# Performance work log

Hardware: AMD Instinct MI355X
Metric: run time of the kernel (lower is better)

Reference implementation:

```python
import jax, jax.numpy as jnp
from jax import lax
import numpy as np

T, B, I, H, OUT = 1024, 32, 128, 512, 10


def _lstm_layer(x, W_ih, W_hh, b):
    """PyTorch-convention LSTM layer. x: [T,B,in], W_ih: [4H,in], W_hh: [4H,H], b: [4H].
    Gate order: i, f, g, o. Returns all hidden states [T,B,H]."""
    hdim = W_hh.shape[1]
    # Precompute input projections for all timesteps (big GEMM, compute-bound).
    x_proj = jnp.einsum('tbi,gi->tbg', x, W_ih) + b  # [T,B,4H]

    def step(carry, xp_t):
        h, c = carry
        gates = xp_t + h @ W_hh.T  # [B,4H]
        i_g, f_g, g_g, o_g = jnp.split(gates, 4, axis=-1)
        i_g = jax.nn.sigmoid(i_g)
        f_g = jax.nn.sigmoid(f_g)
        g_g = jnp.tanh(g_g)
        o_g = jax.nn.sigmoid(o_g)
        c = f_g * c + i_g * g_g
        h = o_g * jnp.tanh(c)
        return (h, c), h

    h0 = jnp.zeros((x.shape[1], hdim), x.dtype)
    c0 = jnp.zeros((x.shape[1], hdim), x.dtype)
    _, hs = lax.scan(step, (h0, c0), x_proj)
    return hs  # [T,B,H]


def setup_inputs() -> dict:
    key = jax.random.key(0)
    ks = jax.random.split(key, 9)
    s1 = 1.0 / np.sqrt(H)  # PyTorch LSTM init scale U(-1/sqrt(H), 1/sqrt(H)); use scaled normal
    return {
        'data': jax.random.normal(ks[0], (T, B, I), jnp.float32),
        'W_ih1': jax.random.normal(ks[1], (4 * H, I), jnp.float32) * s1,
        'W_hh1': jax.random.normal(ks[2], (4 * H, H), jnp.float32) * s1,
        'b1': jax.random.normal(ks[3], (4 * H,), jnp.float32) * s1,
        'W_ih2': jax.random.normal(ks[4], (4 * H, H), jnp.float32) * s1,
        'W_hh2': jax.random.normal(ks[5], (4 * H, H), jnp.float32) * s1,
        'b2': jax.random.normal(ks[6], (4 * H,), jnp.float32) * s1,
        'W3': jax.random.normal(ks[7], (OUT, H), jnp.float32) * s1,
        'b3': jax.random.normal(ks[8], (OUT,), jnp.float32) * s1,
    }


def reference(data, W_ih1, W_hh1, b1, W_ih2, W_hh2, b2, W3, b3):
    h = _lstm_layer(data, W_ih1, W_hh1, b1)   # [T,B,H]
    h = _lstm_layer(h, W_ih2, W_hh2, b2)      # [T,B,H]
    logits = jnp.einsum('tbh,oh->tbo', h, W3) + b3  # [T,B,OUT]
    return jax.nn.softmax(logits, axis=2)
```

## Files before the change

### kernel.cpp

```cpp
#include <hip/hip_runtime.h>
#include <cstdint>
#include <cstddef>

#define TCHUNK 128
#define NCHUNK 8
#define BATCH 32
#define IDIM 128
#define HDIM 512
#define GDIM 2048
#define ODIM 10
#define NBLK 256
#define XPSTEP (GDIM * BATCH)
#define SLAB_F 16384
#define SLAB_B (SLAB_F * 4)

typedef float f4 __attribute__((ext_vector_type(4)));
typedef float f2 __attribute__((ext_vector_type(2)));

__device__ __forceinline__ void llc_store(float* p, float v) {
  asm volatile("global_store_dword %0, %1, off sc0 sc1" :: "v"(p), "v"(v) : "memory");
}
__device__ __forceinline__ float quad_sum(float x) {
  int t = __builtin_amdgcn_update_dpp(0, __float_as_int(x), 0xB1, 0xF, 0xF, true);
  x += __int_as_float(t);
  t = __builtin_amdgcn_update_dpp(0, __float_as_int(x), 0x4E, 0xF, 0xF, true);
  x += __int_as_float(t);
  return x;
}

#define BARRIER() do {                                                      \
    asm volatile("s_waitcnt lgkmcnt(0)" ::: "memory");                      \
    __builtin_amdgcn_sched_barrier(0);                                      \
    __builtin_amdgcn_s_barrier();                                           \
    __builtin_amdgcn_sched_barrier(0);                                      \
  } while (0)

template<int K>
__launch_bounds__(256, 2)
__global__ void proj_kernel(const float* __restrict__ X,
                            const float* __restrict__ W,
                            const float* __restrict__ bias,
                            float* __restrict__ P) {
  __shared__ float Xs[8][132];
  __shared__ float Ws[8][132];
  const int tid = threadIdx.x;
  const int n0 = blockIdx.x * 128;
  const int m0 = blockIdx.y * 128;
  const int tx = tid & 15, ty = tid >> 4;
  const int lm = tid >> 1;
  const int kq = (tid & 1) * 4;
  f2 acc2[8][4];
#pragma unroll
  for (int i = 0; i < 8; ++i)
#pragma unroll
    for (int j = 0; j < 4; ++j) acc2[i][j] = (f2){0.f, 0.f};

  for (int k0 = 0; k0 < K; k0 += 8) {
    const float4 xv = *(const float4*)&X[(size_t)(m0 + lm) * K + k0 + kq];
    const float4 wv = *(const float4*)&W[(size_t)(n0 + lm) * K + k0 + kq];
    __syncthreads();
    Xs[kq + 0][lm] = xv.x; Xs[kq + 1][lm] = xv.y; Xs[kq + 2][lm] = xv.z; Xs[kq + 3][lm] = xv.w;
    Ws[kq + 0][lm] = wv.x; Ws[kq + 1][lm] = wv.y; Ws[kq + 2][lm] = wv.z; Ws[kq + 3][lm] = wv.w;
    __syncthreads();
#pragma unroll
    for (int kk = 0; kk < 8; ++kk) {
      float a[8];
      *(float4*)&a[0] = *(const float4*)&Xs[kk][ty * 8];
      *(float4*)&a[4] = *(const float4*)&Xs[kk][ty * 8 + 4];
      f2 b2[4];
#pragma unroll
      for (int jp = 0; jp < 4; ++jp) b2[jp] = *(const f2*)&Ws[kk][tx * 8 + 2 * jp];
#pragma unroll
      for (int i = 0; i < 8; ++i)
#pragma unroll
        for (int jp = 0; jp < 4; ++jp) acc2[i][jp] += b2[jp] * a[i];
    }
  }
  const int mb = m0 + ty * 8;
  const int t  = mb >> 5;
  const int b0 = mb & 31;
#pragma unroll
  for (int j = 0; j < 8; ++j) {
    const int n = n0 + tx * 8 + j;
    const float bj = bias[n];
    float* dst = &P[((size_t)t * GDIM + n) * BATCH + b0];
#pragma unroll
    for (int i = 0; i < 8; ++i)
      dst[i] = ((j & 1) ? acc2[i][j >> 1].y : acc2[i][j >> 1].x) + bj;
  }
}

__launch_bounds__(256, 1)
__global__ void scan_kernel(const float* __restrict__ xp,
                            const float* __restrict__ Whh,
                            float* __restrict__ hout,
                            float* __restrict__ hb,
                            float* __restrict__ ccur,
                            int first) {
  __shared__ float h_s[2048];
  __shared__ float red[1024];
  __shared__ float pad[17408];

  const int tid = threadIdx.x, bid = blockIdx.x;
  const int g = bid & 7, rank = bid >> 3, slot16 = rank * 16;
  const int w = tid >> 6, l = tid & 63;
  const int s4 = l & 3, rq = l >> 2;
  const int sg = 4 * w + s4;
  const int kb = 32 * sg;

  float wreg[4][32];
#pragma unroll
  for (int r = 0; r < 4; ++r) {
    const int rl = 4 * rq + r;
    const float* wp = Whh + (size_t)((rl >> 4) * HDIM + slot16 + (rl & 15)) * HDIM + kb;
#pragma unroll
    for (int q8 = 0; q8 < 8; ++q8) {
      const f4 v = *(const f4*)&wp[q8 * 4];
      wreg[r][q8 * 4 + 0] = v.x; wreg[r][q8 * 4 + 1] = v.y;
      wreg[r][q8 * 4 + 2] = v.z; wreg[r][q8 * 4 + 3] = v.w;
    }
  }

  const int cl = l >> 4, m = l & 15;
  const int sgS = 4 * w + (m >> 2);
  int dsaddr[8];
#pragma unroll
  for (int i = 0; i < 8; ++i) {
    const int kk = 8 * (m & 3) + i;
    dsaddr[i] = 128 * sgS + ((4 * kk + 8 * sgS) & 127) + cl;
  }
  const int srcoff = cl * 512 + 128 * w + 8 * m;

  const int jj = l >> 2, bb = l & 3;
  const float* xq = xp + (size_t)(slot16 + jj) * BATCH + g * 4 + bb;

  float c_st = 0.f;
  if (!first && w == 0) c_st = ccur[(size_t)(g * 4 + bb) * HDIM + slot16 + jj];

  const int hb0 = 128 * sg;
  const int rot = (8 * sg) & 127;

#pragma unroll 1
  for (int tt = 0; tt < TCHUNK; ++tt) {
    float xq4[4];
    if (w == 0) {
#pragma unroll
      for (int q = 0; q < 4; ++q)
        xq4[q] = xq[(size_t)tt * XPSTEP + q * (HDIM * BATCH)];
    }
    const float* src = hb + (size_t)tt * SLAB_F + g * 2048 + srcoff;
    f4 va, vb;
    int guard = 0;
    while (true) {
      asm volatile("global_load_dwordx4 %0, %2, off sc0 sc1\n\t"
                   "global_load_dwordx4 %1, %3, off sc0 sc1\n\t"
                   "s_waitcnt vmcnt(0)"
                   : "=&v"(va), "=&v"(vb) : "v"(src), "v"(src + 4) : "memory");
      const bool ok =
          __float_as_uint(va.x) != 0xFFFFFFFFu && __float_as_uint(va.y) != 0xFFFFFFFFu &&
          __float_as_uint(va.z) != 0xFFFFFFFFu && __float_as_uint(va.w) != 0xFFFFFFFFu &&
          __float_as_uint(vb.x) != 0xFFFFFFFFu && __float_as_uint(vb.y) != 0xFFFFFFFFu &&
          __float_as_uint(vb.z) != 0xFFFFFFFFu && __float_as_uint(vb.w) != 0xFFFFFFFFu;
      if (__all(ok) || ++guard > 100000) break;
      __builtin_amdgcn_s_sleep(1);
    }
    h_s[dsaddr[0]] = va.x; h_s[dsaddr[1]] = va.y;
    h_s[dsaddr[2]] = va.z; h_s[dsaddr[3]] = va.w;
    h_s[dsaddr[4]] = vb.x; h_s[dsaddr[5]] = vb.y;
    h_s[dsaddr[6]] = vb.z; h_s[dsaddr[7]] = vb.w;
    BARRIER();

    f2 a01[4], a23[4];
#pragma unroll
    for (int r = 0; r < 4; ++r) { a01[r] = (f2){0.f, 0.f}; a23[r] = (f2){0.f, 0.f}; }
#pragma unroll
    for (int kk = 0; kk < 32; ++kk) {
      const f4 hv = *(const f4*)&h_s[hb0 + ((4 * kk + rot) & 127)];
      const f2 h01 = {hv.x, hv.y}, h23 = {hv.z, hv.w};
#pragma unroll
      for (int r = 0; r < 4; ++r) {
        a01[r] += h01 * wreg[r][kk];
        a23[r] += h23 * wreg[r][kk];
      }
    }
#pragma unroll
    for (int r = 0; r < 4; ++r) {
      a01[r].x = quad_sum(a01[r].x); a01[r].y = quad_sum(a01[r].y);
      a23[r].x = quad_sum(a23[r].x); a23[r].y = quad_sum(a23[r].y);
    }
    f2 r01, r23;
    { const f2 v0 = (s4 & 1) ? a01[1] : a01[0];
      const f2 v1 = (s4 & 1) ? a01[3] : a01[2];
      r01 = (s4 & 2) ? v1 : v0;
      const f2 u0 = (s4 & 1) ? a23[1] : a23[0];
      const f2 u1 = (s4 & 1) ? a23[3] : a23[2];
      r23 = (s4 & 2) ? u1 : u0; }
    *(f4*)&red[(w << 8) + 4 * l] = (f4){r01.x, r01.y, r23.x, r23.y};
    BARRIER();

    if (w == 0) {
      float pre[4];
#pragma unroll
      for (int q = 0; q < 4; ++q) {
        const int ri = 4 * (16 * q + jj) + bb;
        pre[q] = red[ri] + red[256 + ri] + red[512 + ri] + red[768 + ri] + xq4[q];
      }
      const float ig = 1.f / (1.f + __expf(-pre[0]));
      const float fg = 1.f / (1.f + __expf(-pre[1]));
      const float gg = tanhf(pre[2]);
      const float og = 1.f / (1.f + __expf(-pre[3]));
      c_st = fg * c_st + ig * gg;
      const float hval = og * tanhf(c_st);
      llc_store(hb + (size_t)(tt + 1) * SLAB_F + g * 2048 + bb * 512 + slot16 + jj, hval);
      hout[(size_t)tt * (BATCH * HDIM) + (size_t)(g * 4 + bb) * HDIM + slot16 + jj] = hval;
    }
  }
  if (w == 0) ccur[(size_t)(g * 4 + bb) * HDIM + slot16 + jj] = c_st;
  ((volatile float*)pad)[tid] = c_st;
}

__launch_bounds__(256, 2)
__global__ void head_kernel(const float* __restrict__ h2,
                            const float* __restrict__ W3,
                            const float* __restrict__ b3,
                            float* __restrict__ outp) {
  const int tid = threadIdx.x;
  const int lane = tid & 63;
  const int wv = tid >> 6;
  const int row = blockIdx.x * 4 + wv;
  const float* hrow = &h2[(size_t)row * HDIM];
  float hreg[8];
  *(float4*)&hreg[0] = *(const float4*)&hrow[lane * 8];
  *(float4*)&hreg[4] = *(const float4*)&hrow[lane * 8 + 4];
  float logit[ODIM];
#pragma unroll
  for (int o = 0; o < ODIM; ++o) {
    const float* wrow = &W3[o * HDIM + lane * 8];
    float w[8];
    *(float4*)&w[0] = *(const float4*)&wrow[0];
    *(float4*)&w[4] = *(const float4*)&wrow[4];
    float pp = 0.f;
#pragma unroll
    for (int j = 0; j < 8; ++j) pp += hreg[j] * w[j];
#pragma unroll
    for (int off = 32; off > 0; off >>= 1) pp += __shfl_xor(pp, off);
    logit[o] = pp + b3[o];
  }
  float mx = logit[0];
#pragma unroll
  for (int o = 1; o < ODIM; ++o) mx = fmaxf(mx, logit[o]);
  float ssum = 0.f;
#pragma unroll
  for (int o = 0; o < ODIM; ++o) { logit[o] = __expf(logit[o] - mx); ssum += logit[o]; }
  const float inv = 1.f / ssum;
  if (lane == 0) {
    float* dst = &outp[(size_t)row * ODIM];
#pragma unroll
    for (int o = 0; o < ODIM; ++o) dst[o] = logit[o] * inv;
  }
}

extern "C" void kernel_launch(void* const* d_in, const int* in_sizes, int n_in,
                              void* d_out, int out_size, void* d_ws, size_t ws_size,
                              hipStream_t stream) {
  const float* data  = (const float*)d_in[0];
  const float* W_ih1 = (const float*)d_in[1];
  const float* W_hh1 = (const float*)d_in[2];
  const float* b1    = (const float*)d_in[3];
  const float* W_ih2 = (const float*)d_in[4];
  const float* W_hh2 = (const float*)d_in[5];
  const float* b2    = (const float*)d_in[6];
  const float* W3    = (const float*)d_in[7];
  const float* b3    = (const float*)d_in[8];
  float* outp = (float*)d_out;

  char* ws = (char*)d_ws;
  size_t off = 0;
  float* xp    = (float*)(ws + off); off += (size_t)TCHUNK * GDIM * BATCH * 4;
  float* h1c   = (float*)(ws + off); off += (size_t)TCHUNK * BATCH * HDIM * 4;
  float* h2c   = (float*)(ws + off); off += (size_t)TCHUNK * BATCH * HDIM * 4;
  float* hb1   = (float*)(ws + off); off += (size_t)(TCHUNK + 1) * SLAB_B;
  float* hb2   = (float*)(ws + off); off += (size_t)(TCHUNK + 1) * SLAB_B;
  float* ccur1 = (float*)(ws + off); off += BATCH * HDIM * 4;
  float* ccur2 = (float*)(ws + off); off += BATCH * HDIM * 4;
  if (off > ws_size) return;

  hipMemsetAsync(hb1, 0x00, SLAB_B, stream);
  hipMemsetAsync((char*)hb1 + SLAB_B, 0xFF, (size_t)TCHUNK * SLAB_B, stream);
  hipMemsetAsync(hb2, 0x00, SLAB_B, stream);
  hipMemsetAsync((char*)hb2 + SLAB_B, 0xFF, (size_t)TCHUNK * SLAB_B, stream);

  const dim3 pgrid(GDIM / 128, (TCHUNK * BATCH) / 128);
  for (int c = 0; c < NCHUNK; ++c) {
    const float* xin = data + (size_t)c * TCHUNK * BATCH * IDIM;
    proj_kernel<IDIM><<<pgrid, 256, 0, stream>>>(xin, W_ih1, b1, xp);
    scan_kernel<<<NBLK, 256, 0, stream>>>(xp, W_hh1, h1c, hb1, ccur1, c == 0);
    if (c < NCHUNK - 1) {
      hipMemcpyAsync(hb1, (char*)hb1 + (size_t)TCHUNK * SLAB_B, SLAB_B,
                     hipMemcpyDeviceToDevice, stream);
      hipMemsetAsync((char*)hb1 + SLAB_B, 0xFF, (size_t)TCHUNK * SLAB_B, stream);
    }
    proj_kernel<HDIM><<<pgrid, 256, 0, stream>>>(h1c, W_ih2, b2, xp);
    scan_kernel<<<NBLK, 256, 0, stream>>>(xp, W_hh2, h2c, hb2, ccur2, c == 0);
    if (c < NCHUNK - 1) {
      hipMemcpyAsync(hb2, (char*)hb2 + (size_t)TCHUNK * SLAB_B, SLAB_B,
                     hipMemcpyDeviceToDevice, stream);
      hipMemsetAsync((char*)hb2 + SLAB_B, 0xFF, (size_t)TCHUNK * SLAB_B, stream);
    }
    head_kernel<<<(TCHUNK * BATCH) / 4, 256, 0, stream>>>(
        h2c, W3, b3, outp + (size_t)c * TCHUNK * BATCH * ODIM);
  }
}
```

Measured before the change: 9.204 ms.

## Remove cross-wave reduction barrier via per-wave k-split and double-buffered h tile

Reassigns work so each wave owns whole hidden units and reduces its k-split partial sums with DPP shuffles inside the wave, dropping the shared-memory reduction buffer and one block barrier per timestep. The h tile in LDS is double-buffered with an XOR swizzle, so only one barrier per step remains. Gate math runs redundantly on all waves using exp-based tanh. The exp-based tanh may lose accuracy or overflow for large inputs, and the redundant gate math adds some ALU work.

```diff
diff --git a/kernel.cpp b/kernel.cpp
--- a/kernel.cpp
+++ b/kernel.cpp
@@ -26,6 +26,19 @@
   t = __builtin_amdgcn_update_dpp(0, __float_as_int(x), 0x4E, 0xF, 0xF, true);
   x += __int_as_float(t);
   return x;
+}
+__device__ __forceinline__ float ror16_sum(float x) {
+  int t = __builtin_amdgcn_update_dpp(0, __float_as_int(x), 0x124, 0xF, 0xF, true);
+  x += __int_as_float(t);
+  t = __builtin_amdgcn_update_dpp(0, __float_as_int(x), 0x128, 0xF, 0xF, true);
+  x += __int_as_float(t);
+  return x;
+}
+__device__ __forceinline__ float fast_sig(float x) {
+  return 1.f / (1.f + __expf(-x));
+}
+__device__ __forceinline__ float fast_tanh(float x) {
+  return 2.f / (1.f + __expf(-2.f * x)) - 1.f;
 }
 
 #define BARRIER() do {                                                      \
@@ -97,58 +110,48 @@
                             float* __restrict__ hb,
                             float* __restrict__ ccur,
                             int first) {
-  __shared__ float h_s[2048];
-  __shared__ float red[1024];
-  __shared__ float pad[17408];
+  __shared__ float h_s[2][2048];
+  __shared__ float pad[16640];
 
   const int tid = threadIdx.x, bid = blockIdx.x;
   const int g = bid & 7, rank = bid >> 3, slot16 = rank * 16;
   const int w = tid >> 6, l = tid & 63;
-  const int s4 = l & 3, rq = l >> 2;
-  const int sg = 4 * w + s4;
-  const int kb = 32 * sg;
+  const int rg = l >> 4, qt = (l >> 2) & 3, sub = l & 3;
+  const int sgn = 4 * qt + sub;
+  const int kb = 32 * sgn;
+  const int slot = slot16 + 4 * w + rg;
+  const int bxk = (16 * sub) ^ (64 * (qt & 1));
 
   float wreg[4][32];
 #pragma unroll
-  for (int r = 0; r < 4; ++r) {
-    const int rl = 4 * rq + r;
-    const float* wp = Whh + (size_t)((rl >> 4) * HDIM + slot16 + (rl & 15)) * HDIM + kb;
+  for (int q = 0; q < 4; ++q) {
+    const float* wp = Whh + (size_t)(q * HDIM + slot) * HDIM + kb;
 #pragma unroll
     for (int q8 = 0; q8 < 8; ++q8) {
       const f4 v = *(const f4*)&wp[q8 * 4];
-      wreg[r][q8 * 4 + 0] = v.x; wreg[r][q8 * 4 + 1] = v.y;
-      wreg[r][q8 * 4 + 2] = v.z; wreg[r][q8 * 4 + 3] = v.w;
+      wreg[q][q8 * 4 + 0] = v.x; wreg[q][q8 * 4 + 1] = v.y;
+      wreg[q][q8 * 4 + 2] = v.z; wreg[q][q8 * 4 + 3] = v.w;
     }
   }
 
   const int cl = l >> 4, m = l & 15;
   const int sgS = 4 * w + (m >> 2);
-  int dsaddr[8];
+  const int bxkS = (16 * (sgS & 3)) ^ (64 * ((sgS >> 2) & 1));
+  int dsb[8];
 #pragma unroll
   for (int i = 0; i < 8; ++i) {
     const int kk = 8 * (m & 3) + i;
-    dsaddr[i] = 128 * sgS + ((4 * kk + 8 * sgS) & 127) + cl;
+    dsb[i] = (512 * sgS) ^ (16 * kk) ^ bxkS | (4 * cl);
   }
   const int srcoff = cl * 512 + 128 * w + 8 * m;
 
-  const int jj = l >> 2, bb = l & 3;
-  const float* xq = xp + (size_t)(slot16 + jj) * BATCH + g * 4 + bb;
+  const float* xq = xp + (size_t)slot * BATCH + g * 4 + sub;
 
   float c_st = 0.f;
-  if (!first && w == 0) c_st = ccur[(size_t)(g * 4 + bb) * HDIM + slot16 + jj];
-
-  const int hb0 = 128 * sg;
-  const int rot = (8 * sg) & 127;
-
-#pragma unroll 1
-  for (int tt = 0; tt < TCHUNK; ++tt) {
-    float xq4[4];
-    if (w == 0) {
-#pragma unroll
-      for (int q = 0; q < 4; ++q)
-        xq4[q] = xq[(size_t)tt * XPSTEP + q * (HDIM * BATCH)];
-    }
-    const float* src = hb + (size_t)tt * SLAB_F + g * 2048 + srcoff;
+  if (!first) c_st = ccur[(size_t)(g * 4 + sub) * HDIM + slot];
+
+  {
+    const float* src = hb + g * 2048 + srcoff;
     f4 va, vb;
     int guard = 0;
     while (true) {
@@ -164,58 +167,82 @@
       if (__all(ok) || ++guard > 100000) break;
       __builtin_amdgcn_s_sleep(1);
     }
-    h_s[dsaddr[0]] = va.x; h_s[dsaddr[1]] = va.y;
-    h_s[dsaddr[2]] = va.z; h_s[dsaddr[3]] = va.w;
-    h_s[dsaddr[4]] = vb.x; h_s[dsaddr[5]] = vb.y;
-    h_s[dsaddr[6]] = vb.z; h_s[dsaddr[7]] = vb.w;
-    BARRIER();
-
+    char* hs0 = (char*)&h_s[0][0];
+    *(float*)(hs0 + dsb[0]) = va.x; *(float*)(hs0 + dsb[1]) = va.y;
+    *(float*)(hs0 + dsb[2]) = va.z; *(float*)(hs0 + dsb[3]) = va.w;
+    *(float*)(hs0 + dsb[4]) = vb.x; *(float*)(hs0 + dsb[5]) = vb.y;
+    *(float*)(hs0 + dsb[6]) = vb.z; *(float*)(hs0 + dsb[7]) = vb.w;
+  }
+  BARRIER();
+
+#pragma unroll 1
+  for (int tt = 0; tt < TCHUNK; ++tt) {
+    float xq4[4];
+#pragma unroll
+    for (int q = 0; q < 4; ++q)
+      xq4[q] = xq[(size_t)tt * XPSTEP + (size_t)q * (HDIM * BATCH)];
+
+    const unsigned sbase = (unsigned)(8192 * (tt & 1) + 512 * sgn) ^ (unsigned)bxk;
+    const char* hsb = (const char*)&h_s[0][0];
     f2 a01[4], a23[4];
 #pragma unroll
-    for (int r = 0; r < 4; ++r) { a01[r] = (f2){0.f, 0.f}; a23[r] = (f2){0.f, 0.f}; }
+    for (int q = 0; q < 4; ++q) { a01[q] = (f2){0.f, 0.f}; a23[q] = (f2){0.f, 0.f}; }
 #pragma unroll
     for (int kk = 0; kk < 32; ++kk) {
-      const f4 hv = *(const f4*)&h_s[hb0 + ((4 * kk + rot) & 127)];
+      const f4 hv = *(const f4*)(hsb + (sbase ^ (unsigned)(16 * kk)));
       const f2 h01 = {hv.x, hv.y}, h23 = {hv.z, hv.w};
 #pragma unroll
-      for (int r = 0; r < 4; ++r) {
-        a01[r] += h01 * wreg[r][kk];
-        a23[r] += h23 * wreg[r][kk];
+      for (int q = 0; q < 4; ++q) {
+        a01[q] += h01 * wreg[q][kk];
+        a23[q] += h23 * wreg[q][kk];
       }
     }
-#pragma unroll
-    for (int r = 0; r < 4; ++r) {
-      a01[r].x = quad_sum(a01[r].x); a01[r].y = quad_sum(a01[r].y);
-      a23[r].x = quad_sum(a23[r].x); a23[r].y = quad_sum(a23[r].y);
-    }
-    f2 r01, r23;
-    { const f2 v0 = (s4 & 1) ? a01[1] : a01[0];
-      const f2 v1 = (s4 & 1) ? a01[3] : a01[2];
-      r01 = (s4 & 2) ? v1 : v0;
-      const f2 u0 = (s4 & 1) ? a23[1] : a23[0];
-      const f2 u1 = (s4 & 1) ? a23[3] : a23[2];
-      r23 = (s4 & 2) ? u1 : u0; }
-    *(f4*)&red[(w << 8) + 4 * l] = (f4){r01.x, r01.y, r23.x, r23.y};
-    BARRIER();
-
-    if (w == 0) {
-      float pre[4];
-#pragma unroll
-      for (int q = 0; q < 4; ++q) {
-        const int ri = 4 * (16 * q + jj) + bb;
-        pre[q] = red[ri] + red[256 + ri] + red[512 + ri] + red[768 + ri] + xq4[q];
+    float pre[4];
+#pragma unroll
+    for (int q = 0; q < 4; ++q) {
+      const f2 p01 = { quad_sum(a01[q].x), quad_sum(a01[q].y) };
+      const f2 p23 = { quad_sum(a23[q].x), quad_sum(a23[q].y) };
+      const f2 ab = (sub & 2) ? p23 : p01;
+      const float sel = (sub & 1) ? ab.y : ab.x;
+      pre[q] = ror16_sum(sel) + xq4[q];
+    }
+    const float ig = fast_sig(pre[0]);
+    const float fg = fast_sig(pre[1]);
+    const float gg = fast_tanh(pre[2]);
+    const float og = fast_sig(pre[3]);
+    c_st = fg * c_st + ig * gg;
+    const float hval = og * fast_tanh(c_st);
+    if (qt == 0) {
+      llc_store(hb + (size_t)(tt + 1) * SLAB_F + g * 2048 + sub * 512 + slot, hval);
+      hout[(size_t)tt * (BATCH * HDIM) + (size_t)(g * 4 + sub) * HDIM + slot] = hval;
+    }
+
+    if (tt + 1 < TCHUNK) {
+      const float* src = hb + (size_t)(tt + 1) * SLAB_F + g * 2048 + srcoff;
+      f4 va, vb;
+      int guard = 0;
+      while (true) {
+        asm volatile("global_load_dwordx4 %0, %2, off sc0 sc1\n\t"
+                     "global_load_dwordx4 %1, %3, off sc0 sc1\n\t"
+                     "s_waitcnt vmcnt(0)"
+                     : "=&v"(va), "=&v"(vb) : "v"(src), "v"(src + 4) : "memory");
+        const bool ok =
+            __float_as_uint(va.x) != 0xFFFFFFFFu && __float_as_uint(va.y) != 0xFFFFFFFFu &&
+            __float_as_uint(va.z) != 0xFFFFFFFFu && __float_as_uint(va.w) != 0xFFFFFFFFu &&
+            __float_as_uint(vb.x) != 0xFFFFFFFFu && __float_as_uint(vb.y) != 0xFFFFFFFFu &&
+            __float_as_uint(vb.z) != 0xFFFFFFFFu && __float_as_uint(vb.w) != 0xFFFFFFFFu;
+        if (__all(ok) || ++guard > 100000) break;
+        __builtin_amdgcn_s_sleep(1);
       }
-      const float ig = 1.f / (1.f + __expf(-pre[0]));
-      const float fg = 1.f / (1.f + __expf(-pre[1]));
-      const float gg = tanhf(pre[2]);
-      const float og = 1.f / (1.f + __expf(-pre[3]));
-      c_st = fg * c_st + ig * gg;
-      const float hval = og * tanhf(c_st);
-      llc_store(hb + (size_t)(tt + 1) * SLAB_F + g * 2048 + bb * 512 + slot16 + jj, hval);
-      hout[(size_t)tt * (BATCH * HDIM) + (size_t)(g * 4 + bb) * HDIM + slot16 + jj] = hval;
-    }
-  }
-  if (w == 0) ccur[(size_t)(g * 4 + bb) * HDIM + slot16 + jj] = c_st;
+      char* hsd = (char*)&h_s[0][0] + 8192 * ((tt + 1) & 1);
+      *(float*)(hsd + dsb[0]) = va.x; *(float*)(hsd + dsb[1]) = va.y;
+      *(float*)(hsd + dsb[2]) = va.z; *(float*)(hsd + dsb[3]) = va.w;
+      *(float*)(hsd + dsb[4]) = vb.x; *(float*)(hsd + dsb[5]) = vb.y;
+      *(float*)(hsd + dsb[6]) = vb.z; *(float*)(hsd + dsb[7]) = vb.w;
+      BARRIER();
+    }
+  }
+  if (qt == 0) ccur[(size_t)(g * 4 + sub) * HDIM + slot] = c_st;
   ((volatile float*)pad)[tid] = c_st;
 }
 
```

Result: slower. 13.86 ms (+50.6%).

## Make each wave own whole gate rows to drop block barriers in LSTM scan

Applied to the files above, without the earlier changes.

Work in the recurrent scan kernel is redistributed so each wavefront loads the full hidden-state slice into its own LDS region and computes complete gate sums for its own hidden slots. The cross-wave LDS reduction and both block-level barriers per timestep are replaced by DPP lane shuffles within a 16-lane group. Each wave now loads 8 dwordx4 per lane instead of 2, so polling traffic from L2 grows fourfold in exchange for removing the inter-wave synchronisation. Gate nonlinearities run in 4 lanes of every wave, where before they ran only in wave 0.

```diff
diff --git a/kernel.cpp b/kernel.cpp
--- a/kernel.cpp
+++ b/kernel.cpp
@@ -20,20 +20,18 @@
 __device__ __forceinline__ void llc_store(float* p, float v) {
   asm volatile("global_store_dword %0, %1, off sc0 sc1" :: "v"(p), "v"(v) : "memory");
 }
-__device__ __forceinline__ float quad_sum(float x) {
-  int t = __builtin_amdgcn_update_dpp(0, __float_as_int(x), 0xB1, 0xF, 0xF, true);
-  x += __int_as_float(t);
-  t = __builtin_amdgcn_update_dpp(0, __float_as_int(x), 0x4E, 0xF, 0xF, true);
-  x += __int_as_float(t);
-  return x;
-}
-
-#define BARRIER() do {                                                      \
-    asm volatile("s_waitcnt lgkmcnt(0)" ::: "memory");                      \
-    __builtin_amdgcn_sched_barrier(0);                                      \
-    __builtin_amdgcn_s_barrier();                                           \
-    __builtin_amdgcn_sched_barrier(0);                                      \
-  } while (0)
+__device__ __forceinline__ float dpp_xor1(float x) {
+  return __int_as_float(__builtin_amdgcn_update_dpp(0, __float_as_int(x), 0xB1, 0xF, 0xF, true));
+}
+__device__ __forceinline__ float dpp_xor2(float x) {
+  return __int_as_float(__builtin_amdgcn_update_dpp(0, __float_as_int(x), 0x4E, 0xF, 0xF, true));
+}
+__device__ __forceinline__ float dpp_ror4(float x) {
+  return __int_as_float(__builtin_amdgcn_update_dpp(0, __float_as_int(x), 0x124, 0xF, 0xF, true));
+}
+__device__ __forceinline__ float dpp_ror8(float x) {
+  return __int_as_float(__builtin_amdgcn_update_dpp(0, __float_as_int(x), 0x128, 0xF, 0xF, true));
+}
 
 template<int K>
 __launch_bounds__(256, 2)
@@ -97,125 +95,145 @@
                             float* __restrict__ hb,
                             float* __restrict__ ccur,
                             int first) {
-  __shared__ float h_s[2048];
-  __shared__ float red[1024];
-  __shared__ float pad[17408];
+  __shared__ float h_all[4][2112];
+  __shared__ float pad[12288];
 
   const int tid = threadIdx.x, bid = blockIdx.x;
   const int g = bid & 7, rank = bid >> 3, slot16 = rank * 16;
   const int w = tid >> 6, l = tid & 63;
-  const int s4 = l & 3, rq = l >> 2;
-  const int sg = 4 * w + s4;
-  const int kb = 32 * sg;
+  const int rg = l >> 4, s16 = l & 15;
+  const int slot = slot16 + 4 * w + rg;
 
   float wreg[4][32];
 #pragma unroll
-  for (int r = 0; r < 4; ++r) {
-    const int rl = 4 * rq + r;
-    const float* wp = Whh + (size_t)((rl >> 4) * HDIM + slot16 + (rl & 15)) * HDIM + kb;
+  for (int q = 0; q < 4; ++q) {
+    const float* wp = Whh + (size_t)(q * HDIM + slot) * HDIM + 32 * s16;
 #pragma unroll
     for (int q8 = 0; q8 < 8; ++q8) {
       const f4 v = *(const f4*)&wp[q8 * 4];
-      wreg[r][q8 * 4 + 0] = v.x; wreg[r][q8 * 4 + 1] = v.y;
-      wreg[r][q8 * 4 + 2] = v.z; wreg[r][q8 * 4 + 3] = v.w;
-    }
-  }
-
-  const int cl = l >> 4, m = l & 15;
-  const int sgS = 4 * w + (m >> 2);
-  int dsaddr[8];
-#pragma unroll
-  for (int i = 0; i < 8; ++i) {
-    const int kk = 8 * (m & 3) + i;
-    dsaddr[i] = 128 * sgS + ((4 * kk + 8 * sgS) & 127) + cl;
-  }
-  const int srcoff = cl * 512 + 128 * w + 8 * m;
-
-  const int jj = l >> 2, bb = l & 3;
-  const float* xq = xp + (size_t)(slot16 + jj) * BATCH + g * 4 + bb;
+      wreg[q][q8 * 4 + 0] = v.x; wreg[q][q8 * 4 + 1] = v.y;
+      wreg[q][q8 * 4 + 2] = v.z; wreg[q][q8 * 4 + 3] = v.w;
+    }
+  }
+
+  const int cl = rg, m = s16;
+  float* hw = &h_all[w][132 * m + cl];
+  const float* hr = &h_all[w][132 * s16];
+  const int srcoff = cl * 512 + 32 * m;
+
+  const int c0 = s16 & 3;
+  const size_t xqo = (size_t)slot * BATCH + g * 4 + c0;
+  const size_t cco = (size_t)(g * 4 + c0) * HDIM + slot;
 
   float c_st = 0.f;
-  if (!first && w == 0) c_st = ccur[(size_t)(g * 4 + bb) * HDIM + slot16 + jj];
-
-  const int hb0 = 128 * sg;
-  const int rot = (8 * sg) & 127;
+  if (!first && s16 < 4) c_st = ccur[cco];
+
+  const int p1 = s16 & 1, p2 = (s16 >> 1) & 1;
 
 #pragma unroll 1
   for (int tt = 0; tt < TCHUNK; ++tt) {
-    float xq4[4];
-    if (w == 0) {
-#pragma unroll
-      for (int q = 0; q < 4; ++q)
-        xq4[q] = xq[(size_t)tt * XPSTEP + q * (HDIM * BATCH)];
-    }
+    __builtin_amdgcn_sched_barrier(0);
     const float* src = hb + (size_t)tt * SLAB_F + g * 2048 + srcoff;
-    f4 va, vb;
+    f4 v0, v1, v2, v3, v4, v5, v6, v7;
     int guard = 0;
     while (true) {
-      asm volatile("global_load_dwordx4 %0, %2, off sc0 sc1\n\t"
-                   "global_load_dwordx4 %1, %3, off sc0 sc1\n\t"
-                   "s_waitcnt vmcnt(0)"
-                   : "=&v"(va), "=&v"(vb) : "v"(src), "v"(src + 4) : "memory");
+      asm volatile(
+          "global_load_dwordx4 %0, %8, off sc0 sc1\n\t"
+          "global_load_dwordx4 %1, %8, off offset:16 sc0 sc1\n\t"
+          "global_load_dwordx4 %2, %8, off offset:32 sc0 sc1\n\t"
+          "global_load_dwordx4 %3, %8, off offset:48 sc0 sc1\n\t"
+          "global_load_dwordx4 %4, %8, off offset:64 sc0 sc1\n\t"
+          "global_load_dwordx4 %5, %8, off offset:80 sc0 sc1\n\t"
+          "global_load_dwordx4 %6, %8, off offset:96 sc0 sc1\n\t"
+          "global_load_dwordx4 %7, %8, off offset:112 sc0 sc1\n\t"
+          "s_waitcnt vmcnt(0)"
+          : "=&v"(v0), "=&v"(v1), "=&v"(v2), "=&v"(v3),
+            "=&v"(v4), "=&v"(v5), "=&v"(v6), "=&v"(v7)
+          : "v"(src) : "memory");
+      unsigned acc = 0xFFFFFFFFu;
+#define CHK(V) acc &= (__float_as_uint(V.x) ^ 0xFFFFFFFFu) | (__float_as_uint(V.y) ^ 0xFFFFFFFFu), \
+               acc &= (__float_as_uint(V.z) ^ 0xFFFFFFFFu) | (__float_as_uint(V.w) ^ 0xFFFFFFFFu)
+#undef CHK
       const bool ok =
-          __float_as_uint(va.x) != 0xFFFFFFFFu && __float_as_uint(va.y) != 0xFFFFFFFFu &&
-          __float_as_uint(va.z) != 0xFFFFFFFFu && __float_as_uint(va.w) != 0xFFFFFFFFu &&
-          __float_as_uint(vb.x) != 0xFFFFFFFFu && __float_as_uint(vb.y) != 0xFFFFFFFFu &&
-          __float_as_uint(vb.z) != 0xFFFFFFFFu && __float_as_uint(vb.w) != 0xFFFFFFFFu;
-      if (__all(ok) || ++guard > 100000) break;
+          __float_as_uint(v0.x) != 0xFFFFFFFFu && __float_as_uint(v0.y) != 0xFFFFFFFFu &&
+          __float_as_uint(v0.z) != 0xFFFFFFFFu && __float_as_uint(v0.w) != 0xFFFFFFFFu &&
+          __float_as_uint(v1.x) != 0xFFFFFFFFu && __float_as_uint(v1.y) != 0xFFFFFFFFu &&
+          __float_as_uint(v1.z) != 0xFFFFFFFFu && __float_as_uint(v1.w) != 0xFFFFFFFFu &&
+          __float_as_uint(v2.x) != 0xFFFFFFFFu && __float_as_uint(v2.y) != 0xFFFFFFFFu &&
+          __float_as_uint(v2.z) != 0xFFFFFFFFu && __float_as_uint(v2.w) != 0xFFFFFFFFu &&
+          __float_as_uint(v3.x) != 0xFFFFFFFFu && __float_as_uint(v3.y) != 0xFFFFFFFFu &&
+          __float_as_uint(v3.z) != 0xFFFFFFFFu && __float_as_uint(v3.w) != 0xFFFFFFFFu &&
+          __float_as_uint(v4.x) != 0xFFFFFFFFu && __float_as_uint(v4.y) != 0xFFFFFFFFu &&
+          __float_as_uint(v4.z) != 0xFFFFFFFFu && __float_as_uint(v4.w) != 0xFFFFFFFFu &&
+          __float_as_uint(v5.x) != 0xFFFFFFFFu && __float_as_uint(v5.y) != 0xFFFFFFFFu &&
+          __float_as_uint(v5.z) != 0xFFFFFFFFu && __float_as_uint(v5.w) != 0xFFFFFFFFu &&
+          __float_as_uint(v6.x) != 0xFFFFFFFFu && __float_as_uint(v6.y) != 0xFFFFFFFFu &&
+          __float_as_uint(v6.z) != 0xFFFFFFFFu && __float_as_uint(v6.w) != 0xFFFFFFFFu &&
+          __float_as_uint(v7.x) != 0xFFFFFFFFu && __float_as_uint(v7.y) != 0xFFFFFFFFu &&
+          __float_as_uint(v7.z) != 0xFFFFFFFFu && __float_as_uint(v7.w) != 0xFFFFFFFFu;
+      if (__all(ok) || ++guard > 200000) break;
       __builtin_amdgcn_s_sleep(1);
     }
-    h_s[dsaddr[0]] = va.x; h_s[dsaddr[1]] = va.y;
-    h_s[dsaddr[2]] = va.z; h_s[dsaddr[3]] = va.w;
-    h_s[dsaddr[4]] = vb.x; h_s[dsaddr[5]] = vb.y;
-    h_s[dsaddr[6]] = vb.z; h_s[dsaddr[7]] = vb.w;
-    BARRIER();
+    __builtin_amdgcn_sched_barrier(0);
+#define PUT(I, V) hw[16*(I) + 0] = V.x; hw[16*(I) + 4] = V.y; \
+                  hw[16*(I) + 8] = V.z; hw[16*(I) + 12] = V.w;
+    PUT(0, v0) PUT(1, v1) PUT(2, v2) PUT(3, v3)
+    PUT(4, v4) PUT(5, v5) PUT(6, v6) PUT(7, v7)
+#undef PUT
+    asm volatile("s_waitcnt lgkmcnt(0)" ::: "memory");
+    __builtin_amdgcn_sched_barrier(0);
 
     f2 a01[4], a23[4];
 #pragma unroll
-    for (int r = 0; r < 4; ++r) { a01[r] = (f2){0.f, 0.f}; a23[r] = (f2){0.f, 0.f}; }
+    for (int q = 0; q < 4; ++q) { a01[q] = (f2){0.f, 0.f}; a23[q] = (f2){0.f, 0.f}; }
 #pragma unroll
     for (int kk = 0; kk < 32; ++kk) {
-      const f4 hv = *(const f4*)&h_s[hb0 + ((4 * kk + rot) & 127)];
+      const f4 hv = *(const f4*)&hr[4 * kk];
       const f2 h01 = {hv.x, hv.y}, h23 = {hv.z, hv.w};
 #pragma unroll
-      for (int r = 0; r < 4; ++r) {
-        a01[r] += h01 * wreg[r][kk];
-        a23[r] += h23 * wreg[r][kk];
+      for (int q = 0; q < 4; ++q) {
+        a01[q] += h01 * wreg[q][kk];
+        a23[q] += h23 * wreg[q][kk];
       }
     }
-#pragma unroll
-    for (int r = 0; r < 4; ++r) {
-      a01[r].x = quad_sum(a01[r].x); a01[r].y = quad_sum(a01[r].y);
-      a23[r].x = quad_sum(a23[r].x); a23[r].y = quad_sum(a23[r].y);
-    }
-    f2 r01, r23;
-    { const f2 v0 = (s4 & 1) ? a01[1] : a01[0];
-      const f2 v1 = (s4 & 1) ? a01[3] : a01[2];
-      r01 = (s4 & 2) ? v1 : v0;
-      const f2 u0 = (s4 & 1) ? a23[1] : a23[0];
-      const f2 u1 = (s4 & 1) ? a23[3] : a23[2];
-      r23 = (s4 & 2) ? u1 : u0; }
-    *(f4*)&red[(w << 8) + 4 * l] = (f4){r01.x, r01.y, r23.x, r23.y};
-    BARRIER();
-
-    if (w == 0) {
-      float pre[4];
-#pragma unroll
-      for (int q = 0; q < 4; ++q) {
-        const int ri = 4 * (16 * q + jj) + bb;
-        pre[q] = red[ri] + red[256 + ri] + red[512 + ri] + red[768 + ri] + xq4[q];
-      }
-      const float ig = 1.f / (1.f + __expf(-pre[0]));
-      const float fg = 1.f / (1.f + __expf(-pre[1]));
-      const float gg = tanhf(pre[2]);
-      const float og = 1.f / (1.f + __expf(-pre[3]));
+    __builtin_amdgcn_sched_barrier(0);
+
+    float k0v[4], k1v[4];
+#pragma unroll
+    for (int q = 0; q < 4; ++q) {
+      const float keep0 = p1 ? a01[q].y : a01[q].x;
+      const float send0 = p1 ? a01[q].x : a01[q].y;
+      const float keep1 = p1 ? a23[q].y : a23[q].x;
+      const float send1 = p1 ? a23[q].x : a23[q].y;
+      k0v[q] = keep0 + dpp_xor1(send0);
+      k1v[q] = keep1 + dpp_xor1(send1);
+    }
+    float bqv[4];
+#pragma unroll
+    for (int q = 0; q < 4; ++q) {
+      const float keep = p2 ? k1v[q] : k0v[q];
+      const float send = p2 ? k0v[q] : k1v[q];
+      bqv[q] = keep + dpp_xor2(send);
+    }
+#pragma unroll
+    for (int q = 0; q < 4; ++q) {
+      bqv[q] += dpp_ror4(bqv[q]);
+      bqv[q] += dpp_ror8(bqv[q]);
+    }
+
+    if (s16 < 4) {
+      const float* xb = xp + (size_t)tt * XPSTEP + xqo;
+      const float ig = 1.f / (1.f + __expf(-(bqv[0] + xb[0])));
+      const float fg = 1.f / (1.f + __expf(-(bqv[1] + xb[(size_t)HDIM * BATCH])));
+      const float gg = tanhf(bqv[2] + xb[(size_t)2 * HDIM * BATCH]);
+      const float og = 1.f / (1.f + __expf(-(bqv[3] + xb[(size_t)3 * HDIM * BATCH])));
       c_st = fg * c_st + ig * gg;
       const float hval = og * tanhf(c_st);
-      llc_store(hb + (size_t)(tt + 1) * SLAB_F + g * 2048 + bb * 512 + slot16 + jj, hval);
-      hout[(size_t)tt * (BATCH * HDIM) + (size_t)(g * 4 + bb) * HDIM + slot16 + jj] = hval;
-    }
-  }
-  if (w == 0) ccur[(size_t)(g * 4 + bb) * HDIM + slot16 + jj] = c_st;
+      llc_store(hb + (size_t)(tt + 1) * SLAB_F + g * 2048 + c0 * 512 + slot, hval);
+      hout[(size_t)tt * (BATCH * HDIM) + (size_t)(g * 4 + c0) * HDIM + slot] = hval;
+    }
+  }
+  if (s16 < 4) ccur[cco] = c_st;
   ((volatile float*)pad)[tid] = c_st;
 }
 
```

After: 26.04 ms. 2.83x slower.
